# Kernel optimization log

Measured on AMD Instinct MI355X. Metric: run time of the kernel, lower is better.

## Reference

```python
import jax, jax.numpy as jnp
import numpy as np

N = 100000   # nodes
R = 3        # relation types (num_edge_type)
E = 600000   # edges per relation -> Etot = 1.8M
C = 2        # num_channels
L = 2        # num_layers (GTConv stack / metapath length)
IN = 64      # in_dim
H = 64       # hidden_dim
K = 50       # num_class
NEG_SLOPE = 0.2  # DGL GATConv default leaky_relu slope


def setup_inputs() -> dict:
    key = jax.random.key(0)
    ks = jax.random.split(key, 12)
    Etot = R * E
    src = jax.random.randint(ks[0], (Etot,), 0, N)
    dst = jax.random.randint(ks[1], (Etot,), 0, N)
    rel = jnp.repeat(jnp.arange(R), E)  # relation id per edge
    h = jax.random.normal(ks[2], (N, IN), jnp.float32)
    # per-channel input projections (fastGTN self.params, xavier-ish)
    params = jax.random.normal(ks[3], (C, IN, H), jnp.float32) * (1.0 / np.sqrt(IN))
    # GTConv weights, one [C, R] filter per layer (init std=0.01)
    gt_w = jax.random.normal(ks[4], (L, C, R), jnp.float32) * 0.01
    # GATConv params: fc (no bias), attn_l, attn_r (num_heads=1)
    fc_w = jax.random.normal(ks[5], (H, H), jnp.float32) * (1.0 / np.sqrt(H))
    attn_l = jax.random.normal(ks[6], (H,), jnp.float32) * 0.1
    attn_r = jax.random.normal(ks[7], (H,), jnp.float32) * 0.1
    # linear_weights: Embedding initialized to 1/top_k, combines channels
    lin_w = jnp.full((C,), 1.0 / C, jnp.float32)
    W2 = jax.random.normal(ks[8], (H, K), jnp.float32) * (1.0 / np.sqrt(H))
    b2 = jnp.zeros((K,), jnp.float32)
    return dict(h=h, params=params, gt_w=gt_w, fc_w=fc_w, attn_l=attn_l,
                attn_r=attn_r, lin_w=lin_w, W2=W2, b2=b2,
                src=src, dst=dst, rel=rel)


def _segment_softmax(logits, seg, n):
    # numerically stable edge softmax over incoming edges of each dst node
    m = jax.ops.segment_max(logits, seg, num_segments=n)
    e = jnp.exp(logits - m[seg])
    s = jax.ops.segment_sum(e, seg, num_segments=n)
    return e / s[seg]


def _gat(src, dst, ft, ew, attn_l, attn_r, n):
    # GATConv_Grad: attention from original ft, then two update_all passes
    el = ft @ attn_l                                   # [N]
    er = ft @ attn_r                                   # [N]
    logits = jax.nn.leaky_relu(el[src] + er[dst], NEG_SLOPE)
    a = _segment_softmax(logits, dst, n)               # [Etot]
    # pass 1: ft <- sum_e ft[src]*edge_weight  (overwrites node frame 'ft')
    ft1 = jax.ops.segment_sum(ft[src] * ew[:, None], dst, num_segments=n)
    # pass 2: ft <- sum_e ft1[src]*a
    ft2 = jax.ops.segment_sum(ft1[src] * a[:, None], dst, num_segments=n)
    return ft2


def reference(h, params, gt_w, fc_w, attn_l, attn_r, lin_w, W2, b2, src, dst, rel):
    n = h.shape[0]
    outs = []
    for c in range(params.shape[0]):           # num_channels (small, fixed)
        Hc = h @ params[c]                     # [N, H]
        for l in range(gt_w.shape[0]):         # num_layers (small, fixed)
            filt = jax.nn.softmax(gt_w[l], axis=-1)     # [C, R] GTConv softmax
            w_e = filt[c][rel]                           # combined relation-graph edge weight
            # EdgeWeightNorm('right'): divide by weighted in-degree at dst
            deg = jax.ops.segment_sum(w_e, dst, num_segments=n)
            w_norm = w_e / jnp.where(deg[dst] > 0, deg[dst], 1.0)
            ft = Hc @ fc_w                               # GAT fc projection
            Hc = _gat(src, dst, ft, w_norm, attn_l, attn_r, n)
        outs.append(Hc)
    Hm = jnp.einsum('c,cnd->nd', lin_w, jnp.stack(outs, 0))  # linear_weights combine
    return Hm @ W2 + b2                        # linear2 -> class logits [N, K]
```

## Files before the change

### kernel.cpp

```cpp
#include <hip/hip_runtime.h>
#include <hip/hip_bf16.h>
#include <math.h>

#define NEG_SLOPE 0.2f
#define NPB_SHIFT 7
#define NPB 128
#define SC_EDGES 16384
#define MAXD 128

__device__ __forceinline__ unsigned bpack(float a, float b) {
    unsigned ua = __float_as_uint(a);
    unsigned ub = __float_as_uint(b);
    ua += 0x7FFFu + ((ua >> 16) & 1u);
    ub += 0x7FFFu + ((ub >> 16) & 1u);
    return (ua >> 16) | (ub & 0xFFFF0000u);
}
__device__ __forceinline__ float2 bunpack(unsigned v) {
    return make_float2(__uint_as_float(v << 16),
                       __uint_as_float(v & 0xFFFF0000u));
}

__global__ void mkfilt(const float* __restrict__ gt_w, float* __restrict__ filt,
                       int rows) {
    int i = threadIdx.x;
    if (i < rows) {
        const float* g = gt_w + i * 3;
        float m = fmaxf(g[0], fmaxf(g[1], g[2]));
        float e0 = __expf(g[0] - m), e1 = __expf(g[1] - m), e2 = __expf(g[2] - m);
        float s = e0 + e1 + e2;
        filt[i * 3 + 0] = e0 / s;
        filt[i * 3 + 1] = e1 / s;
        filt[i * 3 + 2] = e2 / s;
    }
}

__global__ __launch_bounds__(256) void combw_kernel(const float* __restrict__ params,
                                                    const float* __restrict__ fc_w,
                                                    float* __restrict__ WcF) {
    __shared__ __align__(16) float sP[64 * 64], sF[64 * 64];
    const float* P = params + (size_t)blockIdx.x * 64 * 64;
    int t = threadIdx.x;
    for (int i = t * 4; i < 4096; i += 1024) {
        *(float4*)&sP[i] = *(const float4*)&P[i];
        *(float4*)&sF[i] = *(const float4*)&fc_w[i];
    }
    __syncthreads();
    float* O = WcF + (size_t)blockIdx.x * 64 * 64;
    for (int i = t; i < 4096; i += 256) {
        int r = i >> 6, c = i & 63;
        float acc = 0.f;
#pragma unroll
        for (int k = 0; k < 64; ++k) acc += sP[r * 64 + k] * sF[k * 64 + c];
        O[i] = acc;
    }
}

__global__ __launch_bounds__(256) void prep2_kernel(const float* __restrict__ fc_w,
                                                    const float* __restrict__ W2,
                                                    const float* __restrict__ attn_l,
                                                    const float* __restrict__ attn_r,
                                                    float* __restrict__ WfcW2,
                                                    float2* __restrict__ wlr) {
    __shared__ __align__(16) float sF[4096];
    __shared__ float sW[3200], sal[64], sar[64];
    int t = threadIdx.x;
    for (int i = t * 4; i < 4096; i += 1024)
        *(float4*)&sF[i] = *(const float4*)&fc_w[i];
    for (int i = t; i < 3200; i += 256) sW[i] = W2[i];
    if (t < 64) { sal[t] = attn_l[t]; sar[t] = attn_r[t]; }
    __syncthreads();
    if (t < 64) {
        float l = 0.f, r = 0.f;
#pragma unroll
        for (int k = 0; k < 64; ++k) {
            l += sF[t * 64 + k] * sal[k];
            r += sF[t * 64 + k] * sar[k];
        }
        wlr[t] = make_float2(l, r);
    }
    for (int i = t; i < 3200; i += 256) {
        int r = i / 50, c = i - r * 50;
        float acc = 0.f;
#pragma unroll
        for (int k = 0; k < 64; ++k) acc += sF[r * 64 + k] * sW[k * 50 + c];
        WfcW2[i] = acc;
    }
}

__global__ __launch_bounds__(256) void bcount_kernel(const int* __restrict__ dst,
                                                     int* __restrict__ bcnt, int m, int NB) {
    __shared__ int h[1024];
    for (int i = threadIdx.x; i < NB; i += 256) h[i] = 0;
    __syncthreads();
    int base = blockIdx.x * SC_EDGES;
    int endi = base + SC_EDGES; if (endi > m) endi = m;
    for (int i = base + threadIdx.x; i < endi; i += 256)
        atomicAdd(&h[dst[i] >> NPB_SHIFT], 1);
    __syncthreads();
    for (int i = threadIdx.x; i < NB; i += 256)
        if (h[i]) atomicAdd(&bcnt[i], h[i]);
}

__global__ __launch_bounds__(1024) void bscan_kernel(const int* __restrict__ bcnt,
                                                     int* __restrict__ bbase,
                                                     int* __restrict__ bcur, int NB) {
    __shared__ int s[1024];
    int t = threadIdx.x;
    int v = (t < NB) ? bcnt[t] : 0;
    s[t] = v;
    __syncthreads();
    for (int off = 1; off < 1024; off <<= 1) {
        int u = (t >= off) ? s[t - off] : 0;
        __syncthreads();
        s[t] += u;
        __syncthreads();
    }
    if (t < NB) { bbase[t] = s[t] - v; bcur[t] = s[t] - v; }
    if (t == 1023) bbase[NB] = s[1023];
}

__global__ __launch_bounds__(256) void bscatter_kernel(const int* __restrict__ src,
                                                       const int* __restrict__ dst,
                                                       const int* __restrict__ rel,
                                                       int* __restrict__ bcur,
                                                       unsigned* __restrict__ ebuf,
                                                       int m, int NB) {
    __shared__ int cnt[1024];
    for (int i = threadIdx.x; i < NB; i += 256) cnt[i] = 0;
    __syncthreads();
    int base = blockIdx.x * SC_EDGES;
    int endi = base + SC_EDGES; if (endi > m) endi = m;
    for (int i = base + threadIdx.x; i < endi; i += 256)
        atomicAdd(&cnt[dst[i] >> NPB_SHIFT], 1);
    __syncthreads();
    for (int b = threadIdx.x; b < NB; b += 256) {
        int c = cnt[b];
        if (c) cnt[b] = atomicAdd(&bcur[b], c);
    }
    __syncthreads();
    for (int i = base + threadIdx.x; i < endi; i += 256) {
        int d = dst[i];
        int bk = d >> NPB_SHIFT;
        unsigned pk = (unsigned)src[i] | ((unsigned)rel[i] << 17) |
                      ((unsigned)(d & (NPB - 1)) << 19);
        int pos = atomicAdd(&cnt[bk], 1);
        ebuf[pos] = pk;
    }
}

__global__ __launch_bounds__(256) void bfinal_kernel(const unsigned* __restrict__ ebuf,
                                                     const int* __restrict__ bbase,
                                                     int* __restrict__ rowp,
                                                     unsigned* __restrict__ csr,
                                                     int n, int m, int NB) {
    __shared__ int cnt[NPB], cur[NPB], sc[NPB];
    int b = blockIdx.x;
    int t = threadIdx.x;
    int e0 = bbase[b], e1 = bbase[b + 1];
    if (t < NPB) cnt[t] = 0;
    __syncthreads();
    for (int j = e0 + t; j < e1; j += 256)
        atomicAdd(&cnt[(ebuf[j] >> 19) & (NPB - 1)], 1);
    __syncthreads();
    int v0 = (t < NPB) ? cnt[t] : 0;
    if (t < NPB) sc[t] = v0;
    __syncthreads();
    for (int off = 1; off < NPB; off <<= 1) {
        int u = (t >= off && t < NPB) ? sc[t - off] : 0;
        __syncthreads();
        if (t < NPB) sc[t] += u;
        __syncthreads();
    }
    if (t < NPB) {
        int ex = e0 + sc[t] - v0;
        cur[t] = ex;
        int v = b * NPB + t;
        if (v < n) rowp[v] = ex;
    }
    if (b == 0 && t == 0) rowp[n] = m;
    __syncthreads();
    for (int j = e0 + t; j < e1; j += 256) {
        unsigned pk = ebuf[j];
        int dl = (pk >> 19) & (NPB - 1);
        int pos = atomicAdd(&cur[dl], 1);
        csr[pos] = (pk & 0x1FFFF) | (((pk >> 17) & 3) << 20);
    }
}

__global__ __launch_bounds__(256) void gemm_f0(const float* __restrict__ A,
                                               const float* __restrict__ WcF,
                                               unsigned* __restrict__ OAB, int n,
                                               const float* __restrict__ attn_l,
                                               const float* __restrict__ attn_r,
                                               float2* __restrict__ el2,
                                               float2* __restrict__ er2) {
    __shared__ __align__(16) float sW[2][64 * 64];
    __shared__ __align__(16) float sA[64 * 68];
    __shared__ float sAl[64], sAr[64];
    int t = threadIdx.x;
    int row0 = blockIdx.x * 64;
    for (int i = t * 4; i < 8192; i += 1024)
        *(float4*)&sW[0][i] = *(const float4*)&WcF[i];
    if (t < 64) { sAl[t] = attn_l[t]; sAr[t] = attn_r[t]; }
    int rows = n - row0; if (rows > 64) rows = 64;
    for (int i = t * 4; i < 4096; i += 1024) {
        int r = i >> 6, c = i & 63;
        float4 v = {0.f, 0.f, 0.f, 0.f};
        if (r < rows) v = *(const float4*)&A[(size_t)(row0 + r) * 64 + c];
        *(float4*)&sA[r * 68 + c] = v;
    }
    __syncthreads();
    int tr = (t >> 4) * 4, tc = (t & 15) * 4;
    float accA[4][4] = {}, accB[4][4] = {};
#pragma unroll 4
    for (int k = 0; k < 64; k += 4) {
        float4 av[4];
#pragma unroll
        for (int i = 0; i < 4; ++i) av[i] = *(const float4*)&sA[(tr + i) * 68 + k];
#pragma unroll
        for (int kk = 0; kk < 4; ++kk) {
            float4 bA = *(const float4*)&sW[0][(k + kk) * 64 + tc];
            float4 bB = *(const float4*)&sW[1][(k + kk) * 64 + tc];
#pragma unroll
            for (int i = 0; i < 4; ++i) {
                float a = (&av[i].x)[kk];
                accA[i][0] += a * bA.x; accA[i][1] += a * bA.y;
                accA[i][2] += a * bA.z; accA[i][3] += a * bA.w;
                accB[i][0] += a * bB.x; accB[i][1] += a * bB.y;
                accB[i][2] += a * bB.z; accB[i][3] += a * bB.w;
            }
        }
    }
#pragma unroll
    for (int i = 0; i < 4; ++i) {
        int r = row0 + tr + i;
        if (r < n) {
            uint4 v = {bpack(accA[i][0], accB[i][0]), bpack(accA[i][1], accB[i][1]),
                       bpack(accA[i][2], accB[i][2]), bpack(accA[i][3], accB[i][3])};
            *(uint4*)&OAB[(size_t)r * 64 + tc] = v;
        }
    }
    float plA[4], prA[4], plB[4], prB[4];
#pragma unroll
    for (int i = 0; i < 4; ++i) {
        float la = 0.f, ra = 0.f, lb = 0.f, rb = 0.f;
#pragma unroll
        for (int j = 0; j < 4; ++j) {
            la += accA[i][j] * sAl[tc + j]; ra += accA[i][j] * sAr[tc + j];
            lb += accB[i][j] * sAl[tc + j]; rb += accB[i][j] * sAr[tc + j];
        }
        plA[i] = la; prA[i] = ra; plB[i] = lb; prB[i] = rb;
    }
#pragma unroll
    for (int off = 1; off < 16; off <<= 1) {
#pragma unroll
        for (int i = 0; i < 4; ++i) {
            plA[i] += __shfl_xor(plA[i], off); prA[i] += __shfl_xor(prA[i], off);
            plB[i] += __shfl_xor(plB[i], off); prB[i] += __shfl_xor(prB[i], off);
        }
    }
    if ((t & 15) == 0) {
#pragma unroll
        for (int i = 0; i < 4; ++i) {
            int r = row0 + tr + i;
            if (r < n) {
                el2[r] = make_float2(plA[i], plB[i]);
                er2[r] = make_float2(prA[i], prB[i]);
            }
        }
    }
}

__global__ __launch_bounds__(256) void agg1_ab(
        const int* __restrict__ rowp, const unsigned* __restrict__ csr,
        const float* __restrict__ filt, int fo0, int fo1,
        const float2* __restrict__ el, const float2* __restrict__ er,
        const unsigned* __restrict__ ftAB, unsigned* __restrict__ oAB,
        float2* __restrict__ sb, int n) {
    __shared__ unsigned sPk[4][MAXD];
    __shared__ float2 sW2[4][MAXD];
    int w = (blockIdx.x * blockDim.x + threadIdx.x) >> 6;
    int lane = threadIdx.x & 63;
    int wv = threadIdx.x >> 6;
    if (w >= n) return;
    int base = rowp[w], end = rowp[w + 1];
    float fA0 = filt[fo0], fA1 = filt[fo0 + 1], fA2 = filt[fo0 + 2];
    float fB0 = filt[fo1], fB1 = filt[fo1 + 1], fB2 = filt[fo1 + 2];
    float2 erv = er[w];

    float degA = 0.f, degB = 0.f, ssA = 0.f, ssB = 0.f;
    for (int j = base + lane; j < end; j += 64) {
        unsigned pk = csr[j];
        int d = j - base;
        int s = pk & 0x1FFFF;
        int r = pk >> 20;
        float wA = (r == 0) ? fA0 : ((r == 1) ? fA1 : fA2);
        float wB = (r == 0) ? fB0 : ((r == 1) ? fB1 : fB2);
        if (d < MAXD) { sPk[wv][d] = pk; sW2[wv][d] = make_float2(wA, wB); }
        degA += wA; degB += wB;
        float2 e2 = el[s];
        float xA = e2.x + erv.x;
        ssA += __expf(xA > 0.f ? xA : NEG_SLOPE * xA);
        float xB = e2.y + erv.y;
        ssB += __expf(xB > 0.f ? xB : NEG_SLOPE * xB);
    }
    for (int off = 32; off; off >>= 1) {
        degA += __shfl_xor(degA, off); degB += __shfl_xor(degB, off);
        ssA += __shfl_xor(ssA, off);   ssB += __shfl_xor(ssB, off);
    }
    float dA = degA > 0.f ? degA : 1.f;
    float dB = degB > 0.f ? degB : 1.f;

    int deg = end - base;
    int dmax = deg < MAXD ? deg : MAXD;
    float accA = 0.f, accB = 0.f;
    int jj = 0;
    for (; jj + 4 <= dmax; jj += 4) {
        int s0 = sPk[wv][jj] & 0x1FFFF, s1 = sPk[wv][jj + 1] & 0x1FFFF;
        int s2 = sPk[wv][jj + 2] & 0x1FFFF, s3 = sPk[wv][jj + 3] & 0x1FFFF;
        float2 w0 = sW2[wv][jj], w1 = sW2[wv][jj + 1];
        float2 w2 = sW2[wv][jj + 2], w3 = sW2[wv][jj + 3];
        float2 v0 = bunpack(ftAB[(size_t)s0 * 64 + lane]);
        float2 v1 = bunpack(ftAB[(size_t)s1 * 64 + lane]);
        float2 v2 = bunpack(ftAB[(size_t)s2 * 64 + lane]);
        float2 v3 = bunpack(ftAB[(size_t)s3 * 64 + lane]);
        accA += w0.x * v0.x + w1.x * v1.x + w2.x * v2.x + w3.x * v3.x;
        accB += w0.y * v0.y + w1.y * v1.y + w2.y * v2.y + w3.y * v3.y;
    }
    for (; jj < dmax; ++jj) {
        int s = sPk[wv][jj] & 0x1FFFF;
        float2 wv2 = sW2[wv][jj];
        float2 v = bunpack(ftAB[(size_t)s * 64 + lane]);
        accA += wv2.x * v.x;
        accB += wv2.y * v.y;
    }
    for (int j = base + MAXD; j < end; ++j) {
        unsigned pk = csr[j];
        int s = pk & 0x1FFFF;
        int r = pk >> 20;
        float2 v = bunpack(ftAB[(size_t)s * 64 + lane]);
        accA += ((r == 0) ? fA0 : ((r == 1) ? fA1 : fA2)) * v.x;
        accB += ((r == 0) ? fB0 : ((r == 1) ? fB1 : fB2)) * v.y;
    }
    oAB[(size_t)w * 64 + lane] = bpack(accA / dA, accB / dB);
    if (lane == 0)
        sb[w] = make_float2(ssA > 0.f ? 1.f / ssA : 0.f,
                            ssB > 0.f ? 1.f / ssB : 0.f);
}

template <bool EPI>
__global__ __launch_bounds__(256) void agg2_ab(
        const int* __restrict__ rowp, const unsigned* __restrict__ csr,
        const float2* __restrict__ el, const float2* __restrict__ er,
        const float2* __restrict__ sb,
        const unsigned* __restrict__ ftAB, unsigned* __restrict__ oAB,
        const float2* __restrict__ wlr,
        float2* __restrict__ elout, float2* __restrict__ erout, int n) {
    __shared__ unsigned sPk[4][MAXD];
    __shared__ float2 sE[4][MAXD];
    __shared__ float2 sWlr[64];
    int t = threadIdx.x;
    if (EPI) {
        if (t < 64) sWlr[t] = wlr[t];
        __syncthreads();
    }
    int w = (blockIdx.x * blockDim.x + t) >> 6;
    int lane = t & 63;
    int wv = t >> 6;
    if (w >= n) return;
    int base = rowp[w], end = rowp[w + 1];
    float2 erv = er[w];
    float2 inv = sb[w];

    for (int j = base + lane; j < end; j += 64) {
        unsigned pk = csr[j];
        int d = j - base;
        int s = pk & 0x1FFFF;
        float2 e2 = el[s];
        float xA = e2.x + erv.x;
        float xB = e2.y + erv.y;
        float eA = __expf(xA > 0.f ? xA : NEG_SLOPE * xA);
        float eB = __expf(xB > 0.f ? xB : NEG_SLOPE * xB);
        if (d < MAXD) { sPk[wv][d] = pk; sE[wv][d] = make_float2(eA, eB); }
    }

    int deg = end - base;
    int dmax = deg < MAXD ? deg : MAXD;
    float accA = 0.f, accB = 0.f;
    int jj = 0;
    for (; jj + 4 <= dmax; jj += 4) {
        int s0 = sPk[wv][jj] & 0x1FFFF, s1 = sPk[wv][jj + 1] & 0x1FFFF;
        int s2 = sPk[wv][jj + 2] & 0x1FFFF, s3 = sPk[wv][jj + 3] & 0x1FFFF;
        float2 e0 = sE[wv][jj], e1 = sE[wv][jj + 1];
        float2 e2 = sE[wv][jj + 2], e3 = sE[wv][jj + 3];
        float2 v0 = bunpack(ftAB[(size_t)s0 * 64 + lane]);
        float2 v1 = bunpack(ftAB[(size_t)s1 * 64 + lane]);
        float2 v2 = bunpack(ftAB[(size_t)s2 * 64 + lane]);
        float2 v3 = bunpack(ftAB[(size_t)s3 * 64 + lane]);
        accA += e0.x * v0.x + e1.x * v1.x + e2.x * v2.x + e3.x * v3.x;
        accB += e0.y * v0.y + e1.y * v1.y + e2.y * v2.y + e3.y * v3.y;
    }
    for (; jj < dmax; ++jj) {
        int s = sPk[wv][jj] & 0x1FFFF;
        float2 ev = sE[wv][jj];
        float2 v = bunpack(ftAB[(size_t)s * 64 + lane]);
        accA += ev.x * v.x;
        accB += ev.y * v.y;
    }
    for (int j = base + MAXD; j < end; ++j) {
        unsigned pk = csr[j];
        int s = pk & 0x1FFFF;
        float2 e2 = el[s];
        float xA = e2.x + erv.x;
        float xB = e2.y + erv.y;
        float2 v = bunpack(ftAB[(size_t)s * 64 + lane]);
        accA += __expf(xA > 0.f ? xA : NEG_SLOPE * xA) * v.x;
        accB += __expf(xB > 0.f ? xB : NEG_SLOPE * xB) * v.y;
    }
    float oA = accA * inv.x, oB = accB * inv.y;
    oAB[(size_t)w * 64 + lane] = bpack(oA, oB);
    if (EPI) {
        float2 wv2 = sWlr[lane];
        float elA = oA * wv2.x, elB = oB * wv2.x;
        float erA = oA * wv2.y, erB = oB * wv2.y;
        for (int off = 32; off; off >>= 1) {
            elA += __shfl_xor(elA, off); elB += __shfl_xor(elB, off);
            erA += __shfl_xor(erA, off); erB += __shfl_xor(erB, off);
        }
        if (lane == 0) {
            elout[w] = make_float2(elA, elB);
            erout[w] = make_float2(erA, erB);
        }
    }
}

__global__ __launch_bounds__(256) void gemm_out_ab(const unsigned* __restrict__ AAB,
                                                   const float* __restrict__ W,
                                                   const float* __restrict__ b2,
                                                   const float* __restrict__ lin_w,
                                                   float* __restrict__ out, int n) {
    __shared__ __align__(16) float sW[64 * 50];
    __shared__ __align__(16) float sA[64 * 68];
    int t = threadIdx.x;
    int row0 = blockIdx.x * 64;
    float lw0 = lin_w[0], lw1 = lin_w[1];
    for (int i = t; i < 64 * 50; i += 256) sW[i] = W[i];
    int rows = n - row0; if (rows > 64) rows = 64;
    for (int i = t * 4; i < 4096; i += 1024) {
        int r = i >> 6, c = i & 63;
        uint4 v = {0u, 0u, 0u, 0u};
        if (r < rows) v = *(const uint4*)&AAB[(size_t)(row0 + r) * 64 + c];
        float2 f0 = bunpack(v.x), f1 = bunpack(v.y);
        float2 f2 = bunpack(v.z), f3 = bunpack(v.w);
        sA[r * 68 + c]     = lw0 * f0.x + lw1 * f0.y;
        sA[r * 68 + c + 1] = lw0 * f1.x + lw1 * f1.y;
        sA[r * 68 + c + 2] = lw0 * f2.x + lw1 * f2.y;
        sA[r * 68 + c + 3] = lw0 * f3.x + lw1 * f3.y;
    }
    __syncthreads();
    for (int i = t; i < 64 * 50; i += 256) {
        int r = i / 50, col = i - r * 50;
        if (row0 + r >= n) continue;
        float acc = 0.f;
#pragma unroll
        for (int k = 0; k < 64; ++k) acc += sA[r * 68 + k] * sW[k * 50 + col];
        out[(size_t)(row0 + r) * 50 + col] = b2[col] + acc;
    }
}

extern "C" void kernel_launch(void* const* d_in, const int* in_sizes, int n_in,
                              void* d_out, int out_size, void* d_ws, size_t ws_size,
                              hipStream_t stream) {
    const float* h      = (const float*)d_in[0];
    const float* params = (const float*)d_in[1];
    const float* gt_w   = (const float*)d_in[2];
    const float* fc_w   = (const float*)d_in[3];
    const float* attn_l = (const float*)d_in[4];
    const float* attn_r = (const float*)d_in[5];
    const float* lin_w  = (const float*)d_in[6];
    const float* W2     = (const float*)d_in[7];
    const float* b2     = (const float*)d_in[8];
    const int*   src    = (const int*)d_in[9];
    const int*   dst    = (const int*)d_in[10];
    const int*   rel    = (const int*)d_in[11];

    const int n = in_sizes[0] / 64;
    const int m = in_sizes[9];
    const int C = 2, L = 2;
    float* out = (float*)d_out;

    char* base = (char*)d_ws;
    size_t off = 0;
    auto alloc = [&](size_t bytes) -> char* {
        char* p = base + off;
        off = (off + bytes + 255) & ~(size_t)255;
        return p;
    };
    const int NB = (n + NPB - 1) >> NPB_SHIFT;
    const int nchunks = (m + SC_EDGES - 1) / SC_EDGES;
    float*    filt  = (float*)alloc(L * C * 3 * sizeof(float));
    float*    WcF   = (float*)alloc((size_t)C * 64 * 64 * 4);
    float*    WfcW2 = (float*)alloc((size_t)64 * 50 * 4);
    float2*   wlr   = (float2*)alloc((size_t)64 * 8);
    int*      bcnt  = (int*)alloc((size_t)NB * 4);
    int*      bbase = (int*)alloc((size_t)(NB + 1) * 4);
    int*      bcur  = (int*)alloc((size_t)NB * 4);
    int*      rowp  = (int*)alloc((size_t)(n + 1) * 4);
    unsigned* ebuf  = (unsigned*)alloc((size_t)m * 4);
    unsigned* csr   = (unsigned*)alloc((size_t)m * 4);
    float2*   el1   = (float2*)alloc((size_t)n * 8);
    float2*   er1   = (float2*)alloc((size_t)n * 8);
    float2*   elL2  = (float2*)alloc((size_t)n * 8);
    float2*   erL2  = (float2*)alloc((size_t)n * 8);
    float2*   sbAB  = (float2*)alloc((size_t)n * 8);
    unsigned* FAB   = (unsigned*)alloc((size_t)n * 64 * 4);
    unsigned* GAB   = (unsigned*)alloc((size_t)n * 64 * 4);
    unsigned* HAB   = (unsigned*)alloc((size_t)n * 64 * 4);

    hipMemsetAsync(bcnt, 0, (size_t)NB * 4, stream);
    mkfilt<<<1, 64, 0, stream>>>(gt_w, filt, L * C);
    combw_kernel<<<C, 256, 0, stream>>>(params, fc_w, WcF);
    prep2_kernel<<<1, 256, 0, stream>>>(fc_w, W2, attn_l, attn_r, WfcW2, wlr);
    bcount_kernel<<<nchunks, 256, 0, stream>>>(dst, bcnt, m, NB);
    bscan_kernel<<<1, 1024, 0, stream>>>(bcnt, bbase, bcur, NB);
    bscatter_kernel<<<nchunks, 256, 0, stream>>>(src, dst, rel, bcur, ebuf, m, NB);
    bfinal_kernel<<<NB, 256, 0, stream>>>(ebuf, bbase, rowp, csr, n, m, NB);

    const int gB = (n + 63) / 64;
    const int waveBlocks = (n + 3) / 4;

    gemm_f0<<<gB, 256, 0, stream>>>(h, WcF, FAB, n, attn_l, attn_r, el1, er1);
    agg1_ab<<<waveBlocks, 256, 0, stream>>>(rowp, csr, filt, 0, 3,
                                            el1, er1, FAB, GAB, sbAB, n);
    agg2_ab<true><<<waveBlocks, 256, 0, stream>>>(rowp, csr, el1, er1, sbAB,
                                                  GAB, HAB, wlr, elL2, erL2, n);
    agg1_ab<<<waveBlocks, 256, 0, stream>>>(rowp, csr, filt, 6, 9,
                                            elL2, erL2, HAB, GAB, sbAB, n);
    agg2_ab<false><<<waveBlocks, 256, 0, stream>>>(rowp, csr, elL2, erL2, sbAB,
                                                   GAB, HAB, nullptr, nullptr, nullptr, n);
    gemm_out_ab<<<gB, 256, 0, stream>>>(HAB, WfcW2, b2, lin_w, out, n);
}
```

Baseline: 487.3 us.

## Cache per-edge attention exponentials in fp16 buffer and switch features from bf16 to fp16

agg1 now writes the per-edge exp(leaky_relu) values for both channels, packed as half2, into a new edge buffer. agg2 reads them back instead of gathering el[src] and recomputing exp. This replaces a random 8-byte gather per edge with a coalesced 4-byte read, at the cost of an extra 4-byte write per edge in agg1. Feature storage also moves from bf16 to fp16, which risks overflow or lost precision: the unnormalised exponentials and the features are not range-bounded.

```diff
diff --git a/kernel.cpp b/kernel.cpp
--- a/kernel.cpp
+++ b/kernel.cpp
@@ -1,5 +1,6 @@
 #include <hip/hip_runtime.h>
 #include <hip/hip_bf16.h>
+#include <hip/hip_fp16.h>
 #include <math.h>
 
 #define NEG_SLOPE 0.2f
@@ -8,16 +9,13 @@
 #define SC_EDGES 16384
 #define MAXD 128
 
-__device__ __forceinline__ unsigned bpack(float a, float b) {
-    unsigned ua = __float_as_uint(a);
-    unsigned ub = __float_as_uint(b);
-    ua += 0x7FFFu + ((ua >> 16) & 1u);
-    ub += 0x7FFFu + ((ub >> 16) & 1u);
-    return (ua >> 16) | (ub & 0xFFFF0000u);
-}
-__device__ __forceinline__ float2 bunpack(unsigned v) {
-    return make_float2(__uint_as_float(v << 16),
-                       __uint_as_float(v & 0xFFFF0000u));
+__device__ __forceinline__ unsigned hpack(float a, float b) {
+    __half2 h = __floats2half2_rn(a, b);
+    return *(unsigned*)&h;
+}
+__device__ __forceinline__ float2 hunpack(unsigned v) {
+    __half2 h = *(__half2*)&v;
+    return make_float2(__low2float(h), __high2float(h));
 }
 
 __global__ void mkfilt(const float* __restrict__ gt_w, float* __restrict__ filt,
@@ -235,8 +233,8 @@
     for (int i = 0; i < 4; ++i) {
         int r = row0 + tr + i;
         if (r < n) {
-            uint4 v = {bpack(accA[i][0], accB[i][0]), bpack(accA[i][1], accB[i][1]),
-                       bpack(accA[i][2], accB[i][2]), bpack(accA[i][3], accB[i][3])};
+            uint4 v = {hpack(accA[i][0], accB[i][0]), hpack(accA[i][1], accB[i][1]),
+                       hpack(accA[i][2], accB[i][2]), hpack(accA[i][3], accB[i][3])};
             *(uint4*)&OAB[(size_t)r * 64 + tc] = v;
         }
     }
@@ -276,7 +274,7 @@
         const float* __restrict__ filt, int fo0, int fo1,
         const float2* __restrict__ el, const float2* __restrict__ er,
         const unsigned* __restrict__ ftAB, unsigned* __restrict__ oAB,
-        float2* __restrict__ sb, int n) {
+        unsigned* __restrict__ ab, float2* __restrict__ sb, int n) {
     __shared__ unsigned sPk[4][MAXD];
     __shared__ float2 sW2[4][MAXD];
     int w = (blockIdx.x * blockDim.x + threadIdx.x) >> 6;
@@ -300,9 +298,11 @@
         degA += wA; degB += wB;
         float2 e2 = el[s];
         float xA = e2.x + erv.x;
-        ssA += __expf(xA > 0.f ? xA : NEG_SLOPE * xA);
+        float eA = __expf(xA > 0.f ? xA : NEG_SLOPE * xA);
         float xB = e2.y + erv.y;
-        ssB += __expf(xB > 0.f ? xB : NEG_SLOPE * xB);
+        float eB = __expf(xB > 0.f ? xB : NEG_SLOPE * xB);
+        ab[j] = hpack(eA, eB);
+        ssA += eA; ssB += eB;
     }
     for (int off = 32; off; off >>= 1) {
         degA += __shfl_xor(degA, off); degB += __shfl_xor(degB, off);
@@ -320,17 +320,17 @@
         int s2 = sPk[wv][jj + 2] & 0x1FFFF, s3 = sPk[wv][jj + 3] & 0x1FFFF;
         float2 w0 = sW2[wv][jj], w1 = sW2[wv][jj + 1];
         float2 w2 = sW2[wv][jj + 2], w3 = sW2[wv][jj + 3];
-        float2 v0 = bunpack(ftAB[(size_t)s0 * 64 + lane]);
-        float2 v1 = bunpack(ftAB[(size_t)s1 * 64 + lane]);
-        float2 v2 = bunpack(ftAB[(size_t)s2 * 64 + lane]);
-        float2 v3 = bunpack(ftAB[(size_t)s3 * 64 + lane]);
+        float2 v0 = hunpack(ftAB[(size_t)s0 * 64 + lane]);
+        float2 v1 = hunpack(ftAB[(size_t)s1 * 64 + lane]);
+        float2 v2 = hunpack(ftAB[(size_t)s2 * 64 + lane]);
+        float2 v3 = hunpack(ftAB[(size_t)s3 * 64 + lane]);
         accA += w0.x * v0.x + w1.x * v1.x + w2.x * v2.x + w3.x * v3.x;
         accB += w0.y * v0.y + w1.y * v1.y + w2.y * v2.y + w3.y * v3.y;
     }
     for (; jj < dmax; ++jj) {
         int s = sPk[wv][jj] & 0x1FFFF;
         float2 wv2 = sW2[wv][jj];
-        float2 v = bunpack(ftAB[(size_t)s * 64 + lane]);
+        float2 v = hunpack(ftAB[(size_t)s * 64 + lane]);
         accA += wv2.x * v.x;
         accB += wv2.y * v.y;
     }
@@ -338,11 +338,11 @@
         unsigned pk = csr[j];
         int s = pk & 0x1FFFF;
         int r = pk >> 20;
-        float2 v = bunpack(ftAB[(size_t)s * 64 + lane]);
+        float2 v = hunpack(ftAB[(size_t)s * 64 + lane]);
         accA += ((r == 0) ? fA0 : ((r == 1) ? fA1 : fA2)) * v.x;
         accB += ((r == 0) ? fB0 : ((r == 1) ? fB1 : fB2)) * v.y;
     }
-    oAB[(size_t)w * 64 + lane] = bpack(accA / dA, accB / dB);
+    oAB[(size_t)w * 64 + lane] = hpack(accA / dA, accB / dB);
     if (lane == 0)
         sb[w] = make_float2(ssA > 0.f ? 1.f / ssA : 0.f,
                             ssB > 0.f ? 1.f / ssB : 0.f);
@@ -351,8 +351,7 @@
 template <bool EPI>
 __global__ __launch_bounds__(256) void agg2_ab(
         const int* __restrict__ rowp, const unsigned* __restrict__ csr,
-        const float2* __restrict__ el, const float2* __restrict__ er,
-        const float2* __restrict__ sb,
+        const unsigned* __restrict__ ab, const float2* __restrict__ sb,
         const unsigned* __restrict__ ftAB, unsigned* __restrict__ oAB,
         const float2* __restrict__ wlr,
         float2* __restrict__ elout, float2* __restrict__ erout, int n) {
@@ -369,19 +368,14 @@
     int wv = t >> 6;
     if (w >= n) return;
     int base = rowp[w], end = rowp[w + 1];
-    float2 erv = er[w];
     float2 inv = sb[w];
 
     for (int j = base + lane; j < end; j += 64) {
-        unsigned pk = csr[j];
         int d = j - base;
-        int s = pk & 0x1FFFF;
-        float2 e2 = el[s];
-        float xA = e2.x + erv.x;
-        float xB = e2.y + erv.y;
-        float eA = __expf(xA > 0.f ? xA : NEG_SLOPE * xA);
-        float eB = __expf(xB > 0.f ? xB : NEG_SLOPE * xB);
-        if (d < MAXD) { sPk[wv][d] = pk; sE[wv][d] = make_float2(eA, eB); }
+        if (d < MAXD) {
+            sPk[wv][d] = csr[j];
+            sE[wv][d] = hunpack(ab[j]);
+        }
     }
 
     int deg = end - base;
@@ -393,32 +387,30 @@
         int s2 = sPk[wv][jj + 2] & 0x1FFFF, s3 = sPk[wv][jj + 3] & 0x1FFFF;
         float2 e0 = sE[wv][jj], e1 = sE[wv][jj + 1];
         float2 e2 = sE[wv][jj + 2], e3 = sE[wv][jj + 3];
-        float2 v0 = bunpack(ftAB[(size_t)s0 * 64 + lane]);
-        float2 v1 = bunpack(ftAB[(size_t)s1 * 64 + lane]);
-        float2 v2 = bunpack(ftAB[(size_t)s2 * 64 + lane]);
-        float2 v3 = bunpack(ftAB[(size_t)s3 * 64 + lane]);
+        float2 v0 = hunpack(ftAB[(size_t)s0 * 64 + lane]);
+        float2 v1 = hunpack(ftAB[(size_t)s1 * 64 + lane]);
+        float2 v2 = hunpack(ftAB[(size_t)s2 * 64 + lane]);
+        float2 v3 = hunpack(ftAB[(size_t)s3 * 64 + lane]);
         accA += e0.x * v0.x + e1.x * v1.x + e2.x * v2.x + e3.x * v3.x;
         accB += e0.y * v0.y + e1.y * v1.y + e2.y * v2.y + e3.y * v3.y;
     }
     for (; jj < dmax; ++jj) {
         int s = sPk[wv][jj] & 0x1FFFF;
         float2 ev = sE[wv][jj];
-        float2 v = bunpack(ftAB[(size_t)s * 64 + lane]);
+        float2 v = hunpack(ftAB[(size_t)s * 64 + lane]);
         accA += ev.x * v.x;
         accB += ev.y * v.y;
     }
     for (int j = base + MAXD; j < end; ++j) {
         unsigned pk = csr[j];
         int s = pk & 0x1FFFF;
-        float2 e2 = el[s];
-        float xA = e2.x + erv.x;
-        float xB = e2.y + erv.y;
-        float2 v = bunpack(ftAB[(size_t)s * 64 + lane]);
-        accA += __expf(xA > 0.f ? xA : NEG_SLOPE * xA) * v.x;
-        accB += __expf(xB > 0.f ? xB : NEG_SLOPE * xB) * v.y;
+        float2 ev = hunpack(ab[j]);
+        float2 v = hunpack(ftAB[(size_t)s * 64 + lane]);
+        accA += ev.x * v.x;
+        accB += ev.y * v.y;
     }
     float oA = accA * inv.x, oB = accB * inv.y;
-    oAB[(size_t)w * 64 + lane] = bpack(oA, oB);
+    oAB[(size_t)w * 64 + lane] = hpack(oA, oB);
     if (EPI) {
         float2 wv2 = sWlr[lane];
         float elA = oA * wv2.x, elB = oB * wv2.x;
@@ -450,8 +442,8 @@
         int r = i >> 6, c = i & 63;
         uint4 v = {0u, 0u, 0u, 0u};
         if (r < rows) v = *(const uint4*)&AAB[(size_t)(row0 + r) * 64 + c];
-        float2 f0 = bunpack(v.x), f1 = bunpack(v.y);
-        float2 f2 = bunpack(v.z), f3 = bunpack(v.w);
+        float2 f0 = hunpack(v.x), f1 = hunpack(v.y);
+        float2 f2 = hunpack(v.z), f3 = hunpack(v.w);
         sA[r * 68 + c]     = lw0 * f0.x + lw1 * f0.y;
         sA[r * 68 + c + 1] = lw0 * f1.x + lw1 * f1.y;
         sA[r * 68 + c + 2] = lw0 * f2.x + lw1 * f2.y;
@@ -508,6 +500,7 @@
     int*      rowp  = (int*)alloc((size_t)(n + 1) * 4);
     unsigned* ebuf  = (unsigned*)alloc((size_t)m * 4);
     unsigned* csr   = (unsigned*)alloc((size_t)m * 4);
+    unsigned* abuf  = (unsigned*)alloc((size_t)m * 4);
     float2*   el1   = (float2*)alloc((size_t)n * 8);
     float2*   er1   = (float2*)alloc((size_t)n * 8);
     float2*   elL2  = (float2*)alloc((size_t)n * 8);
@@ -531,12 +524,12 @@
 
     gemm_f0<<<gB, 256, 0, stream>>>(h, WcF, FAB, n, attn_l, attn_r, el1, er1);
     agg1_ab<<<waveBlocks, 256, 0, stream>>>(rowp, csr, filt, 0, 3,
-                                            el1, er1, FAB, GAB, sbAB, n);
-    agg2_ab<true><<<waveBlocks, 256, 0, stream>>>(rowp, csr, el1, er1, sbAB,
+                                            el1, er1, FAB, GAB, abuf, sbAB, n);
+    agg2_ab<true><<<waveBlocks, 256, 0, stream>>>(rowp, csr, abuf, sbAB,
                                                   GAB, HAB, wlr, elL2, erL2, n);
     agg1_ab<<<waveBlocks, 256, 0, stream>>>(rowp, csr, filt, 6, 9,
-                                            elL2, erL2, HAB, GAB, sbAB, n);
-    agg2_ab<false><<<waveBlocks, 256, 0, stream>>>(rowp, csr, elL2, erL2, sbAB,
+                                            elL2, erL2, HAB, GAB, abuf, sbAB, n);
+    agg2_ab<false><<<waveBlocks, 256, 0, stream>>>(rowp, csr, abuf, sbAB,
                                                    GAB, HAB, nullptr, nullptr, nullptr, n);
     gemm_out_ab<<<gB, 256, 0, stream>>>(HAB, WfcW2, b2, lin_w, out, n);
 }
```

After: 478.0 us. Within noise of the previous version (-1.9%).
